# Kernel optimization log

Hardware: AMD Instinct MI355X
Metric: run time of the kernel (lower is better)

Reference implementation:

```python
import jax, jax.numpy as jnp
import numpy as np

DIM = 512
HEADS = 8


def setup_inputs() -> dict:
    key = jax.random.key(0)
    ks = jax.random.split(key, 9)
    s = 1.0 / np.sqrt(DIM)
    x = jax.random.normal(ks[0], (2, 4096, DIM), dtype=jnp.float32)
    Wq = jax.random.uniform(ks[1], (DIM, DIM), jnp.float32, -s, s)
    bq = jax.random.uniform(ks[2], (DIM,), jnp.float32, -s, s)
    Wk = jax.random.uniform(ks[3], (DIM, DIM), jnp.float32, -s, s)
    bk = jax.random.uniform(ks[4], (DIM,), jnp.float32, -s, s)
    Wv = jax.random.uniform(ks[5], (DIM, DIM), jnp.float32, -s, s)
    bv = jax.random.uniform(ks[6], (DIM,), jnp.float32, -s, s)
    Wo = jax.random.uniform(ks[7], (DIM, DIM), jnp.float32, -s, s)
    bo = jax.random.uniform(ks[8], (DIM,), jnp.float32, -s, s)
    return {"x": x, "Wq": Wq, "bq": bq, "Wk": Wk, "bk": bk,
            "Wv": Wv, "bv": bv, "Wo": Wo, "bo": bo}


def reference(x, Wq, bq, Wk, bk, Wv, bv, Wo, bo):
    b, t, d = x.shape
    h = HEADS
    dq = d // h
    scale = dq ** -0.5
    # projections: torch Linear is x @ W.T + b
    q = (x @ Wq.T + bq).reshape(b, t, h, dq)
    k = (x @ Wk.T + bk).reshape(b, t, h, dq)
    v = (x @ Wv.T + bv).reshape(b, t, h, dq)
    # attention scores [b, h, t, t] (full O(T^2) matrix, as in the original)
    att = jnp.einsum("bqhd,bkhd->bhqk", q, k) * scale
    att = jax.nn.softmax(att, axis=-1)
    out = jnp.einsum("bhqk,bkhd->bqhd", att, v).reshape(b, t, d)
    return out @ Wo.T + bo
```

## Files before the change

### kernel.cpp

```cpp
#include <hip/hip_runtime.h>

typedef short bf16x8 __attribute__((ext_vector_type(8)));
typedef float f32x4 __attribute__((ext_vector_type(4)));

#define MFMA(a, b, c) __builtin_amdgcn_mfma_f32_16x16x32_bf16((a), (b), (c), 0, 0, 0)

__device__ __forceinline__ unsigned short f2bf(float f) {
    unsigned u = __builtin_bit_cast(unsigned, f);
    unsigned r = u + 0x7FFFu + ((u >> 16) & 1u);
    return (unsigned short)(r >> 16);
}
__device__ __forceinline__ unsigned rne2(float a, float b) {
    unsigned ua = __builtin_bit_cast(unsigned, a);
    unsigned ub = __builtin_bit_cast(unsigned, b);
    ua += 0x7FFFu + ((ua >> 16) & 1u);
    ub += 0x7FFFu + ((ub >> 16) & 1u);
    return __builtin_amdgcn_perm(ub, ua, 0x07060302u);
}

__global__ __launch_bounds__(256) void cvt_kernel(
    const float* __restrict__ x,
    const float* __restrict__ w0, const float* __restrict__ w1,
    const float* __restrict__ w2, const float* __restrict__ w3,
    unsigned short* __restrict__ xd,
    unsigned short* __restrict__ d0, unsigned short* __restrict__ d1,
    unsigned short* __restrict__ d2, unsigned short* __restrict__ d3)
{
    int bid = blockIdx.x;
    const float* src;
    unsigned short* dst;
    int off;
    if (bid < 4096) { src = x; dst = xd; off = bid; }
    else {
        int s = (bid - 4096) >> 8;
        src = s == 0 ? w0 : (s == 1 ? w1 : (s == 2 ? w2 : w3));
        dst = s == 0 ? d0 : (s == 1 ? d1 : (s == 2 ? d2 : d3));
        off = (bid - 4096) & 255;
    }
    size_t i = ((size_t)off * 256 + threadIdx.x) * 4;
    float4 v = *(const float4*)(src + i);
    uint2 pk;
    pk.x = rne2(v.x, v.y);
    pk.y = rne2(v.z, v.w);
    *(uint2*)(dst + i) = pk;
}

__device__ __forceinline__ void gemm128_core(
    const unsigned short* __restrict__ A, const unsigned short* __restrict__ W,
    int m0, int n0, int tid, unsigned short* sA, unsigned short* sB,
    f32x4 acc[4][4])
{
    const int lane = tid & 63, wid = tid >> 6;
    const int quad = lane >> 4, l15 = lane & 15;
    const int wm = wid >> 1, wn = wid & 1;

    #pragma unroll
    for (int i = 0; i < 4; i++)
        #pragma unroll
        for (int j = 0; j < 4; j++) {
            f32x4 z = {0.f, 0.f, 0.f, 0.f};
            acc[i][j] = z;
        }

    for (int k0 = 0; k0 < 512; k0 += 64) {
        #pragma unroll
        for (int p = 0; p < 4; p++) {
            int c = tid + p * 256;
            int row = c >> 3, kc = c & 7;
            uint4 va = *(const uint4*)(A + (size_t)(m0 + row) * 512 + k0 + kc * 8);
            *(uint4*)((char*)sA + row * 128 + ((kc ^ (row & 7)) << 4)) = va;
            uint4 vb = *(const uint4*)(W + (size_t)(n0 + row) * 512 + k0 + kc * 8);
            *(uint4*)((char*)sB + row * 128 + ((kc ^ (row & 7)) << 4)) = vb;
        }
        __syncthreads();
        #pragma unroll
        for (int ks = 0; ks < 2; ks++) {
            bf16x8 af[4], bfr[4];
            #pragma unroll
            for (int i = 0; i < 4; i++) {
                int row = wm * 64 + i * 16 + l15;
                int kc = ks * 4 + quad;
                af[i] = *(const bf16x8*)((const char*)sA + row * 128 + ((kc ^ (row & 7)) << 4));
            }
            #pragma unroll
            for (int j = 0; j < 4; j++) {
                int row = wn * 64 + j * 16 + l15;
                int kc = ks * 4 + quad;
                bfr[j] = *(const bf16x8*)((const char*)sB + row * 128 + ((kc ^ (row & 7)) << 4));
            }
            #pragma unroll
            for (int i = 0; i < 4; i++)
                #pragma unroll
                for (int j = 0; j < 4; j++)
                    acc[i][j] = MFMA(af[i], bfr[j], acc[i][j]);
        }
        __syncthreads();
    }
}

__global__ __launch_bounds__(256) void qkv_kernel(
    const unsigned short* __restrict__ x,
    const unsigned short* __restrict__ Wq, const float* __restrict__ bq,
    const unsigned short* __restrict__ Wk, const float* __restrict__ bk,
    const unsigned short* __restrict__ Wv, const float* __restrict__ bv,
    unsigned short* __restrict__ qo, unsigned short* __restrict__ ko,
    unsigned short* __restrict__ vo)
{
    __shared__ unsigned short sA[128 * 64];
    __shared__ unsigned short sB[128 * 64];
    const int tid = threadIdx.x;
    const int by = blockIdx.y;
    const int sel = by >> 2;
    const int n0 = (by & 3) * 128;
    const int m0 = blockIdx.x * 128;
    const unsigned short* W = sel == 0 ? Wq : (sel == 1 ? Wk : Wv);
    const float* bias = sel == 0 ? bq : (sel == 1 ? bk : bv);

    f32x4 acc[4][4];
    gemm128_core(x, W, m0, n0, tid, sA, sB, acc);

    const int lane = tid & 63, wid = tid >> 6;
    const int quad = lane >> 4, l15 = lane & 15;
    const int wm = wid >> 1, wn = wid & 1;
    float bv4[4];
    #pragma unroll
    for (int j = 0; j < 4; j++) bv4[j] = bias[n0 + wn * 64 + j * 16 + l15];

    if (sel == 2) {
        #pragma unroll
        for (int i = 0; i < 4; i++) {
            #pragma unroll
            for (int j = 0; j < 4; j++) {
                int n = n0 + wn * 64 + j * 16 + l15;
                int h = n >> 6, d = n & 63;
                int m = m0 + wm * 64 + i * 16 + quad * 4;
                int b = m >> 12, t = m & 4095;
                uint2 pk;
                pk.x = rne2(acc[i][j][0] + bv4[j], acc[i][j][1] + bv4[j]);
                pk.y = rne2(acc[i][j][2] + bv4[j], acc[i][j][3] + bv4[j]);
                *(uint2*)(vo + ((size_t)(b * 8 + h) * 64 + d) * 4096 + t) = pk;
            }
        }
    } else {
        const float SC = (sel == 0) ? 0.125f * 1.44269504088896f : 1.0f;
        unsigned short* dst = sel == 0 ? qo : ko;
        #pragma unroll
        for (int i = 0; i < 4; i++) {
            #pragma unroll
            for (int j = 0; j < 4; j++) {
                int n = n0 + wn * 64 + j * 16 + l15;
                int h = n >> 6, d = n & 63;
                #pragma unroll
                for (int r = 0; r < 4; r++) {
                    int m = m0 + wm * 64 + i * 16 + quad * 4 + r;
                    int b = m >> 12, t = m & 4095;
                    dst[((size_t)(b * 8 + h) * 4096 + t) * 64 + d] =
                        f2bf((acc[i][j][r] + bv4[j]) * SC);
                }
            }
        }
    }
}

__global__ __launch_bounds__(512, 4) void attn_kernel(
    const unsigned short* __restrict__ qg, const unsigned short* __restrict__ kg,
    const unsigned short* __restrict__ vtg, unsigned short* __restrict__ og)
{
    __shared__ unsigned char smem[65536];

    const int tid = threadIdx.x;
    const int lane = tid & 63;
    const int w = tid >> 6;
    const int g = tid >> 8;
    const int gt = tid & 255;
    const int sw = w & 3;
    const int quad = lane >> 4, l15 = lane & 15;
    const int bh = blockIdx.y;
    const size_t base = (size_t)bh * 4096 * 64;
    const unsigned short* Q = qg + base;
    const unsigned short* K = kg + base;
    const unsigned short* VT = vtg + base;
    const int qt0 = blockIdx.x * 128;

    unsigned short* sK  = (unsigned short*)(smem + g * 8192);
    unsigned short* sVt = (unsigned short*)(smem + 16384 + g * 8192);
    unsigned char*  sP  = smem + 32768 + w * 4096;

    bf16x8 qf[2][2];
    #pragma unroll
    for (int cb = 0; cb < 2; cb++) {
        int q = qt0 + sw * 32 + cb * 16 + l15;
        #pragma unroll
        for (int ks = 0; ks < 2; ks++)
            qf[cb][ks] = *(const bf16x8*)(Q + (size_t)q * 64 + ks * 32 + quad * 8);
    }

    f32x4 ot[4][2];
    #pragma unroll
    for (int i = 0; i < 4; i++)
        #pragma unroll
        for (int cb = 0; cb < 2; cb++) {
            f32x4 z = {0.f, 0.f, 0.f, 0.f};
            ot[i][cb] = z;
        }
    f32x4 ls[2];
    {
        f32x4 z = {0.f, 0.f, 0.f, 0.f};
        ls[0] = z; ls[1] = z;
    }
    const short one_b = (short)0x3F80;
    const bf16x8 ones = {one_b, one_b, one_b, one_b, one_b, one_b, one_b, one_b};

    const int c0 = gt, c1 = gt + 256;
    const int r0 = c0 >> 3, kc0 = c0 & 7;
    const int r1 = c1 >> 3, kc1 = c1 & 7;

    uint4 kr0, kr1, vr0, vr1;
    {
        int kb = g * 64;
        kr0 = *(const uint4*)(K + (size_t)(kb + r0) * 64 + kc0 * 8);
        kr1 = *(const uint4*)(K + (size_t)(kb + r1) * 64 + kc1 * 8);
        vr0 = *(const uint4*)(VT + (size_t)r0 * 4096 + kb + kc0 * 8);
        vr1 = *(const uint4*)(VT + (size_t)r1 * 4096 + kb + kc1 * 8);
    }

    for (int it = 0; it < 32; it++) {
        *(uint4*)((char*)sK + r0 * 128 + ((kc0 ^ (r0 & 7)) << 4)) = kr0;
        *(uint4*)((char*)sK + r1 * 128 + ((kc1 ^ (r1 & 7)) << 4)) = kr1;
        *(uint4*)((char*)sVt + r0 * 128 + ((kc0 ^ (r0 & 7)) << 4)) = vr0;
        *(uint4*)((char*)sVt + r1 * 128 + ((kc1 ^ (r1 & 7)) << 4)) = vr1;
        __syncthreads();

        {
            int itn = (it < 31) ? it + 1 : it;
            int kbn = (2 * itn + g) * 64;
            kr0 = *(const uint4*)(K + (size_t)(kbn + r0) * 64 + kc0 * 8);
            kr1 = *(const uint4*)(K + (size_t)(kbn + r1) * 64 + kc1 * 8);
            vr0 = *(const uint4*)(VT + (size_t)r0 * 4096 + kbn + kc0 * 8);
            vr1 = *(const uint4*)(VT + (size_t)r1 * 4096 + kbn + kc1 * 8);
        }

        #pragma unroll
        for (int rb = 0; rb < 4; rb++) {
            int row = rb * 16 + l15;
            f32x4 s0 = {0.f, 0.f, 0.f, 0.f};
            f32x4 s1 = {0.f, 0.f, 0.f, 0.f};
            #pragma unroll
            for (int ks = 0; ks < 2; ks++) {
                int kc = ks * 4 + quad;
                bf16x8 ka = *(const bf16x8*)((const char*)sK + row * 128 + ((kc ^ (row & 7)) << 4));
                s0 = MFMA(ka, qf[0][ks], s0);
                s1 = MFMA(ka, qf[1][ks], s1);
            }
            int poff = (((rb * 2 + (quad >> 1)) ^ (l15 & 7)) << 4) + ((quad & 1) << 3);
            {
                float p0 = __builtin_amdgcn_exp2f(s0[0]);
                float p1 = __builtin_amdgcn_exp2f(s0[1]);
                float p2 = __builtin_amdgcn_exp2f(s0[2]);
                float p3 = __builtin_amdgcn_exp2f(s0[3]);
                uint2 pk;
                pk.x = rne2(p0, p1);
                pk.y = rne2(p2, p3);
                *(uint2*)(sP + l15 * 128 + poff) = pk;
            }
            {
                float p0 = __builtin_amdgcn_exp2f(s1[0]);
                float p1 = __builtin_amdgcn_exp2f(s1[1]);
                float p2 = __builtin_amdgcn_exp2f(s1[2]);
                float p3 = __builtin_amdgcn_exp2f(s1[3]);
                uint2 pk;
                pk.x = rne2(p0, p1);
                pk.y = rne2(p2, p3);
                *(uint2*)(sP + (16 + l15) * 128 + poff) = pk;
            }
        }
        __asm__ __volatile__("s_waitcnt lgkmcnt(0)" ::: "memory");

        #pragma unroll
        for (int ks2 = 0; ks2 < 2; ks2++) {
            int pslot = (((ks2 * 4 + quad) ^ (l15 & 7)) << 4);
            bf16x8 pfr0 = *(const bf16x8*)(sP + l15 * 128 + pslot);
            bf16x8 pfr1 = *(const bf16x8*)(sP + (16 + l15) * 128 + pslot);
            ls[0] = MFMA(ones, pfr0, ls[0]);
            ls[1] = MFMA(ones, pfr1, ls[1]);
            #pragma unroll
            for (int rbd = 0; rbd < 4; rbd++) {
                int row = rbd * 16 + l15;
                int kc = ks2 * 4 + quad;
                bf16x8 vf = *(const bf16x8*)((const char*)sVt + row * 128 + ((kc ^ (row & 7)) << 4));
                ot[rbd][0] = MFMA(vf, pfr0, ot[rbd][0]);
                ot[rbd][1] = MFMA(vf, pfr1, ot[rbd][1]);
            }
        }
        __syncthreads();
    }

    float* oc = (float*)(smem + 32768);
    float* lc = (float*)smem;
    if (g == 1) {
        #pragma unroll
        for (int cb = 0; cb < 2; cb++) {
            int qb = sw * 32 + cb * 16 + l15;
            if (quad == 0) lc[qb] = ls[cb][0];
            #pragma unroll
            for (int rbd = 0; rbd < 4; rbd++) {
                int dc = rbd * 4 + quad;
                *(f32x4*)((char*)oc + qb * 256 + ((dc ^ (qb & 15)) << 4)) = ot[rbd][cb];
            }
        }
    }
    __syncthreads();
    if (g == 0) {
        const int b = bh >> 3, h = bh & 7;
        #pragma unroll
        for (int cb = 0; cb < 2; cb++) {
            int qb = sw * 32 + cb * 16 + l15;
            float inv = 1.f / (ls[cb][0] + lc[qb]);
            int q = qt0 + qb;
            #pragma unroll
            for (int rbd = 0; rbd < 4; rbd++) {
                int dc = rbd * 4 + quad;
                f32x4 o2 = *(const f32x4*)((char*)oc + qb * 256 + ((dc ^ (qb & 15)) << 4));
                float v0 = (ot[rbd][cb][0] + o2[0]) * inv;
                float v1 = (ot[rbd][cb][1] + o2[1]) * inv;
                float v2 = (ot[rbd][cb][2] + o2[2]) * inv;
                float v3 = (ot[rbd][cb][3] + o2[3]) * inv;
                uint2 pk;
                pk.x = rne2(v0, v1);
                pk.y = rne2(v2, v3);
                *(uint2*)(og + ((size_t)(b * 4096 + q) * 512 + h * 64 + rbd * 16 + quad * 4)) = pk;
            }
        }
    }
}

__global__ __launch_bounds__(256) void out_kernel(
    const unsigned short* __restrict__ attn,
    const unsigned short* __restrict__ Wo, const float* __restrict__ bo,
    float* __restrict__ out)
{
    __shared__ unsigned short sA[128 * 64];
    __shared__ unsigned short sB[128 * 64];
    const int tid = threadIdx.x;
    const int m0 = blockIdx.x * 128;
    const int n0 = blockIdx.y * 128;

    f32x4 acc[4][4];
    gemm128_core(attn, Wo, m0, n0, tid, sA, sB, acc);

    const int lane = tid & 63, wid = tid >> 6;
    const int quad = lane >> 4, l15 = lane & 15;
    const int wm = wid >> 1, wn = wid & 1;
    float bv4[4];
    #pragma unroll
    for (int j = 0; j < 4; j++) bv4[j] = bo[n0 + wn * 64 + j * 16 + l15];
    #pragma unroll
    for (int i = 0; i < 4; i++) {
        #pragma unroll
        for (int j = 0; j < 4; j++) {
            int n = n0 + wn * 64 + j * 16 + l15;
            #pragma unroll
            for (int r = 0; r < 4; r++) {
                int m = m0 + wm * 64 + i * 16 + quad * 4 + r;
                out[(size_t)m * 512 + n] = acc[i][j][r] + bv4[j];
            }
        }
    }
}

extern "C" void kernel_launch(void* const* d_in, const int* in_sizes, int n_in,
                              void* d_out, int out_size, void* d_ws, size_t ws_size,
                              hipStream_t stream) {
    const float* x  = (const float*)d_in[0];
    const float* Wq = (const float*)d_in[1];
    const float* bq = (const float*)d_in[2];
    const float* Wk = (const float*)d_in[3];
    const float* bk = (const float*)d_in[4];
    const float* Wv = (const float*)d_in[5];
    const float* bv = (const float*)d_in[6];
    const float* Wo = (const float*)d_in[7];
    const float* bo = (const float*)d_in[8];
    unsigned short* ws = (unsigned short*)d_ws;

    const size_t NTOK = (size_t)2 * 4096 * 512;
    const size_t WSZ = (size_t)512 * 512;
    unsigned short* xb  = ws;
    unsigned short* Wqb = ws + NTOK;
    unsigned short* Wkb = Wqb + WSZ;
    unsigned short* Wvb = Wkb + WSZ;
    unsigned short* Wob = Wvb + WSZ;
    unsigned short* q_ws = Wob + WSZ;
    unsigned short* k_ws = q_ws + NTOK;
    unsigned short* v_ws = k_ws + NTOK;
    unsigned short* a_ws = v_ws + NTOK;

    cvt_kernel<<<5120, 256, 0, stream>>>(x, Wq, Wk, Wv, Wo, xb, Wqb, Wkb, Wvb, Wob);
    qkv_kernel<<<dim3(64, 12), 256, 0, stream>>>(xb, Wqb, bq, Wkb, bk, Wvb, bv,
                                                 q_ws, k_ws, v_ws);
    attn_kernel<<<dim3(32, 16), 512, 0, stream>>>(q_ws, k_ws, v_ws, a_ws);
    out_kernel<<<dim3(64, 4), 256, 0, stream>>>(a_ws, Wob, bo,
                                                (float*)d_out);
}
```

Measured before the change: 206.3 us.

## Fuse x fp32-to-bf16 conversion into QKV GEMM and vectorize epilogue stores

```diff
diff --git a/kernel.cpp b/kernel.cpp
--- a/kernel.cpp
+++ b/kernel.cpp
@@ -5,39 +5,40 @@
 
 #define MFMA(a, b, c) __builtin_amdgcn_mfma_f32_16x16x32_bf16((a), (b), (c), 0, 0, 0)
 
-__device__ __forceinline__ unsigned short f2bf(float f) {
-    unsigned u = __builtin_bit_cast(unsigned, f);
-    unsigned r = u + 0x7FFFu + ((u >> 16) & 1u);
-    return (unsigned short)(r >> 16);
-}
 __device__ __forceinline__ unsigned rne2(float a, float b) {
+#if __has_builtin(__builtin_amdgcn_cvt_pk_bf16_f32)
+    auto v = __builtin_amdgcn_cvt_pk_bf16_f32(a, b);
+    return __builtin_bit_cast(unsigned, v);
+#else
     unsigned ua = __builtin_bit_cast(unsigned, a);
     unsigned ub = __builtin_bit_cast(unsigned, b);
     ua += 0x7FFFu + ((ua >> 16) & 1u);
     ub += 0x7FFFu + ((ub >> 16) & 1u);
     return __builtin_amdgcn_perm(ub, ua, 0x07060302u);
+#endif
+}
+
+__device__ __forceinline__ uint4 cvt8(const float* __restrict__ p) {
+    float4 a = *(const float4*)p;
+    float4 b = *(const float4*)(p + 4);
+    uint4 r;
+    r.x = rne2(a.x, a.y);
+    r.y = rne2(a.z, a.w);
+    r.z = rne2(b.x, b.y);
+    r.w = rne2(b.z, b.w);
+    return r;
 }
 
 __global__ __launch_bounds__(256) void cvt_kernel(
-    const float* __restrict__ x,
     const float* __restrict__ w0, const float* __restrict__ w1,
     const float* __restrict__ w2, const float* __restrict__ w3,
-    unsigned short* __restrict__ xd,
     unsigned short* __restrict__ d0, unsigned short* __restrict__ d1,
     unsigned short* __restrict__ d2, unsigned short* __restrict__ d3)
 {
-    int bid = blockIdx.x;
-    const float* src;
-    unsigned short* dst;
-    int off;
-    if (bid < 4096) { src = x; dst = xd; off = bid; }
-    else {
-        int s = (bid - 4096) >> 8;
-        src = s == 0 ? w0 : (s == 1 ? w1 : (s == 2 ? w2 : w3));
-        dst = s == 0 ? d0 : (s == 1 ? d1 : (s == 2 ? d2 : d3));
-        off = (bid - 4096) & 255;
-    }
-    size_t i = ((size_t)off * 256 + threadIdx.x) * 4;
+    int s = blockIdx.x >> 8;
+    const float* src = s == 0 ? w0 : (s == 1 ? w1 : (s == 2 ? w2 : w3));
+    unsigned short* dst = s == 0 ? d0 : (s == 1 ? d1 : (s == 2 ? d2 : d3));
+    size_t i = ((size_t)(blockIdx.x & 255) * 256 + threadIdx.x) * 4;
     float4 v = *(const float4*)(src + i);
     uint2 pk;
     pk.x = rne2(v.x, v.y);
@@ -45,9 +46,10 @@
     *(uint2*)(dst + i) = pk;
 }
 
+template<bool AF32, bool BF32>
 __device__ __forceinline__ void gemm128_core(
-    const unsigned short* __restrict__ A, const unsigned short* __restrict__ W,
-    int m0, int n0, int tid, unsigned short* sA, unsigned short* sB,
+    const void* __restrict__ A, const void* __restrict__ B,
+    int a0, int b0, int tid, unsigned short* sA, unsigned short* sB,
     f32x4 acc[4][4])
 {
     const int lane = tid & 63, wid = tid >> 6;
@@ -67,9 +69,12 @@
         for (int p = 0; p < 4; p++) {
             int c = tid + p * 256;
             int row = c >> 3, kc = c & 7;
-            uint4 va = *(const uint4*)(A + (size_t)(m0 + row) * 512 + k0 + kc * 8);
+            uint4 va, vb;
+            if (AF32) va = cvt8((const float*)A + (size_t)(a0 + row) * 512 + k0 + kc * 8);
+            else      va = *(const uint4*)((const unsigned short*)A + (size_t)(a0 + row) * 512 + k0 + kc * 8);
+            if (BF32) vb = cvt8((const float*)B + (size_t)(b0 + row) * 512 + k0 + kc * 8);
+            else      vb = *(const uint4*)((const unsigned short*)B + (size_t)(b0 + row) * 512 + k0 + kc * 8);
             *(uint4*)((char*)sA + row * 128 + ((kc ^ (row & 7)) << 4)) = va;
-            uint4 vb = *(const uint4*)(W + (size_t)(n0 + row) * 512 + k0 + kc * 8);
             *(uint4*)((char*)sB + row * 128 + ((kc ^ (row & 7)) << 4)) = vb;
         }
         __syncthreads();
@@ -99,7 +104,7 @@
 }
 
 __global__ __launch_bounds__(256) void qkv_kernel(
-    const unsigned short* __restrict__ x,
+    const float* __restrict__ x,
     const unsigned short* __restrict__ Wq, const float* __restrict__ bq,
     const unsigned short* __restrict__ Wk, const float* __restrict__ bk,
     const unsigned short* __restrict__ Wv, const float* __restrict__ bv,
@@ -109,24 +114,22 @@
     __shared__ unsigned short sA[128 * 64];
     __shared__ unsigned short sB[128 * 64];
     const int tid = threadIdx.x;
-    const int by = blockIdx.y;
-    const int sel = by >> 2;
-    const int n0 = (by & 3) * 128;
-    const int m0 = blockIdx.x * 128;
-    const unsigned short* W = sel == 0 ? Wq : (sel == 1 ? Wk : Wv);
-    const float* bias = sel == 0 ? bq : (sel == 1 ? bk : bv);
-
-    f32x4 acc[4][4];
-    gemm128_core(x, W, m0, n0, tid, sA, sB, acc);
+    const int bx = blockIdx.x;
+    const int sel = bx >> 2;
+    const int n0 = (bx & 3) * 128;
+    const int m0 = blockIdx.y * 128;
 
     const int lane = tid & 63, wid = tid >> 6;
     const int quad = lane >> 4, l15 = lane & 15;
     const int wm = wid >> 1, wn = wid & 1;
-    float bv4[4];
-    #pragma unroll
-    for (int j = 0; j < 4; j++) bv4[j] = bias[n0 + wn * 64 + j * 16 + l15];
+
+    f32x4 acc[4][4];
 
     if (sel == 2) {
+        gemm128_core<true, false>(x, Wv, m0, n0, tid, sA, sB, acc);
+        float bv4[4];
+        #pragma unroll
+        for (int j = 0; j < 4; j++) bv4[j] = bv[n0 + wn * 64 + j * 16 + l15];
         #pragma unroll
         for (int i = 0; i < 4; i++) {
             #pragma unroll
@@ -142,21 +145,24 @@
             }
         }
     } else {
+        const unsigned short* W = sel == 0 ? Wq : Wk;
+        const float* bias = sel == 0 ? bq : bk;
+        unsigned short* dst = sel == 0 ? qo : ko;
         const float SC = (sel == 0) ? 0.125f * 1.44269504088896f : 1.0f;
-        unsigned short* dst = sel == 0 ? qo : ko;
+        gemm128_core<false, true>(W, x, n0, m0, tid, sA, sB, acc);
         #pragma unroll
         for (int i = 0; i < 4; i++) {
+            int nb = n0 + wm * 64 + i * 16 + quad * 4;
+            int h = nb >> 6, d0 = nb & 63;
+            f32x4 bb = *(const f32x4*)(bias + nb);
             #pragma unroll
             for (int j = 0; j < 4; j++) {
-                int n = n0 + wn * 64 + j * 16 + l15;
-                int h = n >> 6, d = n & 63;
-                #pragma unroll
-                for (int r = 0; r < 4; r++) {
-                    int m = m0 + wm * 64 + i * 16 + quad * 4 + r;
-                    int b = m >> 12, t = m & 4095;
-                    dst[((size_t)(b * 8 + h) * 4096 + t) * 64 + d] =
-                        f2bf((acc[i][j][r] + bv4[j]) * SC);
-                }
+                int m = m0 + wn * 64 + j * 16 + l15;
+                int b = m >> 12, t = m & 4095;
+                uint2 pk;
+                pk.x = rne2((acc[i][j][0] + bb[0]) * SC, (acc[i][j][1] + bb[1]) * SC);
+                pk.y = rne2((acc[i][j][2] + bb[2]) * SC, (acc[i][j][3] + bb[3]) * SC);
+                *(uint2*)(dst + ((size_t)(b * 8 + h) * 4096 + t) * 64 + d0) = pk;
             }
         }
     }
@@ -342,28 +348,28 @@
     __shared__ unsigned short sA[128 * 64];
     __shared__ unsigned short sB[128 * 64];
     const int tid = threadIdx.x;
-    const int m0 = blockIdx.x * 128;
-    const int n0 = blockIdx.y * 128;
+    const int n0 = blockIdx.x * 128;
+    const int m0 = blockIdx.y * 128;
 
     f32x4 acc[4][4];
-    gemm128_core(attn, Wo, m0, n0, tid, sA, sB, acc);
+    gemm128_core<false, false>(Wo, attn, n0, m0, tid, sA, sB, acc);
 
     const int lane = tid & 63, wid = tid >> 6;
     const int quad = lane >> 4, l15 = lane & 15;
     const int wm = wid >> 1, wn = wid & 1;
-    float bv4[4];
-    #pragma unroll
-    for (int j = 0; j < 4; j++) bv4[j] = bo[n0 + wn * 64 + j * 16 + l15];
     #pragma unroll
     for (int i = 0; i < 4; i++) {
+        int nb = n0 + wm * 64 + i * 16 + quad * 4;
+        f32x4 bb = *(const f32x4*)(bo + nb);
         #pragma unroll
         for (int j = 0; j < 4; j++) {
-            int n = n0 + wn * 64 + j * 16 + l15;
-            #pragma unroll
-            for (int r = 0; r < 4; r++) {
-                int m = m0 + wm * 64 + i * 16 + quad * 4 + r;
-                out[(size_t)m * 512 + n] = acc[i][j][r] + bv4[j];
-            }
+            int m = m0 + wn * 64 + j * 16 + l15;
+            f32x4 v;
+            v[0] = acc[i][j][0] + bb[0];
+            v[1] = acc[i][j][1] + bb[1];
+            v[2] = acc[i][j][2] + bb[2];
+            v[3] = acc[i][j][3] + bb[3];
+            *(f32x4*)(out + (size_t)m * 512 + nb) = v;
         }
     }
 }
@@ -384,8 +390,7 @@
 
     const size_t NTOK = (size_t)2 * 4096 * 512;
     const size_t WSZ = (size_t)512 * 512;
-    unsigned short* xb  = ws;
-    unsigned short* Wqb = ws + NTOK;
+    unsigned short* Wqb = ws;
     unsigned short* Wkb = Wqb + WSZ;
     unsigned short* Wvb = Wkb + WSZ;
     unsigned short* Wob = Wvb + WSZ;
@@ -394,10 +399,10 @@
     unsigned short* v_ws = k_ws + NTOK;
     unsigned short* a_ws = v_ws + NTOK;
 
-    cvt_kernel<<<5120, 256, 0, stream>>>(x, Wq, Wk, Wv, Wo, xb, Wqb, Wkb, Wvb, Wob);
-    qkv_kernel<<<dim3(64, 12), 256, 0, stream>>>(xb, Wqb, bq, Wkb, bk, Wvb, bv,
+    cvt_kernel<<<1024, 256, 0, stream>>>(Wq, Wk, Wv, Wo, Wqb, Wkb, Wvb, Wob);
+    qkv_kernel<<<dim3(12, 64), 256, 0, stream>>>(x, Wqb, bq, Wkb, bk, Wvb, bv,
                                                  q_ws, k_ws, v_ws);
     attn_kernel<<<dim3(32, 16), 512, 0, stream>>>(q_ws, k_ws, v_ws, a_ws);
-    out_kernel<<<dim3(64, 4), 256, 0, stream>>>(a_ws, Wob, bo,
+    out_kernel<<<dim3(4, 64), 256, 0, stream>>>(a_ws, Wob, bo,
                                                 (float*)d_out);
 }
```

Measured after the change: 216.3 us. +4.9%, slower.

## Halve attention block to 4 waves, each covering 64 queries for more K/V reuse

Applied to the files above, without the earlier changes.

```diff
diff --git a/kernel.cpp b/kernel.cpp
--- a/kernel.cpp
+++ b/kernel.cpp
@@ -11,11 +11,16 @@
     return (unsigned short)(r >> 16);
 }
 __device__ __forceinline__ unsigned rne2(float a, float b) {
+#if __has_builtin(__builtin_amdgcn_cvt_pk_bf16_f32)
+    auto v = __builtin_amdgcn_cvt_pk_bf16_f32(a, b);
+    return __builtin_bit_cast(unsigned, v);
+#else
     unsigned ua = __builtin_bit_cast(unsigned, a);
     unsigned ub = __builtin_bit_cast(unsigned, b);
     ua += 0x7FFFu + ((ua >> 16) & 1u);
     ub += 0x7FFFu + ((ub >> 16) & 1u);
     return __builtin_amdgcn_perm(ub, ua, 0x07060302u);
+#endif
 }
 
 __global__ __launch_bounds__(256) void cvt_kernel(
@@ -162,7 +167,7 @@
     }
 }
 
-__global__ __launch_bounds__(512, 4) void attn_kernel(
+__global__ __launch_bounds__(256, 2) void attn_kernel(
     const unsigned short* __restrict__ qg, const unsigned short* __restrict__ kg,
     const unsigned short* __restrict__ vtg, unsigned short* __restrict__ og)
 {
@@ -171,9 +176,8 @@
     const int tid = threadIdx.x;
     const int lane = tid & 63;
     const int w = tid >> 6;
-    const int g = tid >> 8;
-    const int gt = tid & 255;
-    const int sw = w & 3;
+    const int g = w >> 1;
+    const int sw = w & 1;
     const int quad = lane >> 4, l15 = lane & 15;
     const int bh = blockIdx.y;
     const size_t base = (size_t)bh * 4096 * 64;
@@ -184,112 +188,116 @@
 
     unsigned short* sK  = (unsigned short*)(smem + g * 8192);
     unsigned short* sVt = (unsigned short*)(smem + 16384 + g * 8192);
-    unsigned char*  sP  = smem + 32768 + w * 4096;
-
-    bf16x8 qf[2][2];
-    #pragma unroll
-    for (int cb = 0; cb < 2; cb++) {
-        int q = qt0 + sw * 32 + cb * 16 + l15;
+    unsigned char*  sP  = smem + 32768 + w * 8192;
+
+    bf16x8 qf[4][2];
+    #pragma unroll
+    for (int cb = 0; cb < 4; cb++) {
+        int q = qt0 + sw * 64 + cb * 16 + l15;
         #pragma unroll
         for (int ks = 0; ks < 2; ks++)
             qf[cb][ks] = *(const bf16x8*)(Q + (size_t)q * 64 + ks * 32 + quad * 8);
     }
 
-    f32x4 ot[4][2];
+    f32x4 ot[4][4];
     #pragma unroll
     for (int i = 0; i < 4; i++)
         #pragma unroll
-        for (int cb = 0; cb < 2; cb++) {
+        for (int cb = 0; cb < 4; cb++) {
             f32x4 z = {0.f, 0.f, 0.f, 0.f};
             ot[i][cb] = z;
         }
-    f32x4 ls[2];
-    {
+    f32x4 ls[4];
+    #pragma unroll
+    for (int cb = 0; cb < 4; cb++) {
         f32x4 z = {0.f, 0.f, 0.f, 0.f};
-        ls[0] = z; ls[1] = z;
+        ls[cb] = z;
     }
     const short one_b = (short)0x3F80;
     const bf16x8 ones = {one_b, one_b, one_b, one_b, one_b, one_b, one_b, one_b};
 
-    const int c0 = gt, c1 = gt + 256;
-    const int r0 = c0 >> 3, kc0 = c0 & 7;
-    const int r1 = c1 >> 3, kc1 = c1 & 7;
-
-    uint4 kr0, kr1, vr0, vr1;
+    const int r_lo = tid >> 3, r_hi = 32 + (tid >> 3), kc = tid & 7;
+    const int swz_lo = ((kc ^ (r_lo & 7)) << 4);
+
+    uint4 kr0, kr1, kr2, kr3, vr0, vr1, vr2, vr3;
     {
-        int kb = g * 64;
-        kr0 = *(const uint4*)(K + (size_t)(kb + r0) * 64 + kc0 * 8);
-        kr1 = *(const uint4*)(K + (size_t)(kb + r1) * 64 + kc1 * 8);
-        vr0 = *(const uint4*)(VT + (size_t)r0 * 4096 + kb + kc0 * 8);
-        vr1 = *(const uint4*)(VT + (size_t)r1 * 4096 + kb + kc1 * 8);
+        int kb0 = 0, kb1 = 64;
+        kr0 = *(const uint4*)(K + (size_t)(kb0 + r_lo) * 64 + kc * 8);
+        kr1 = *(const uint4*)(K + (size_t)(kb0 + r_hi) * 64 + kc * 8);
+        kr2 = *(const uint4*)(K + (size_t)(kb1 + r_lo) * 64 + kc * 8);
+        kr3 = *(const uint4*)(K + (size_t)(kb1 + r_hi) * 64 + kc * 8);
+        vr0 = *(const uint4*)(VT + (size_t)r_lo * 4096 + kb0 + kc * 8);
+        vr1 = *(const uint4*)(VT + (size_t)r_hi * 4096 + kb0 + kc * 8);
+        vr2 = *(const uint4*)(VT + (size_t)r_lo * 4096 + kb1 + kc * 8);
+        vr3 = *(const uint4*)(VT + (size_t)r_hi * 4096 + kb1 + kc * 8);
     }
 
     for (int it = 0; it < 32; it++) {
-        *(uint4*)((char*)sK + r0 * 128 + ((kc0 ^ (r0 & 7)) << 4)) = kr0;
-        *(uint4*)((char*)sK + r1 * 128 + ((kc1 ^ (r1 & 7)) << 4)) = kr1;
-        *(uint4*)((char*)sVt + r0 * 128 + ((kc0 ^ (r0 & 7)) << 4)) = vr0;
-        *(uint4*)((char*)sVt + r1 * 128 + ((kc1 ^ (r1 & 7)) << 4)) = vr1;
+        *(uint4*)(smem + r_lo * 128 + swz_lo) = kr0;
+        *(uint4*)(smem + r_hi * 128 + swz_lo) = kr1;
+        *(uint4*)(smem + 8192 + r_lo * 128 + swz_lo) = kr2;
+        *(uint4*)(smem + 8192 + r_hi * 128 + swz_lo) = kr3;
+        *(uint4*)(smem + 16384 + r_lo * 128 + swz_lo) = vr0;
+        *(uint4*)(smem + 16384 + r_hi * 128 + swz_lo) = vr1;
+        *(uint4*)(smem + 24576 + r_lo * 128 + swz_lo) = vr2;
+        *(uint4*)(smem + 24576 + r_hi * 128 + swz_lo) = vr3;
         __syncthreads();
 
         {
             int itn = (it < 31) ? it + 1 : it;
-            int kbn = (2 * itn + g) * 64;
-            kr0 = *(const uint4*)(K + (size_t)(kbn + r0) * 64 + kc0 * 8);
-            kr1 = *(const uint4*)(K + (size_t)(kbn + r1) * 64 + kc1 * 8);
-            vr0 = *(const uint4*)(VT + (size_t)r0 * 4096 + kbn + kc0 * 8);
-            vr1 = *(const uint4*)(VT + (size_t)r1 * 4096 + kbn + kc1 * 8);
+            int kb0 = (2 * itn) * 64, kb1 = (2 * itn + 1) * 64;
+            kr0 = *(const uint4*)(K + (size_t)(kb0 + r_lo) * 64 + kc * 8);
+            kr1 = *(const uint4*)(K + (size_t)(kb0 + r_hi) * 64 + kc * 8);
+            kr2 = *(const uint4*)(K + (size_t)(kb1 + r_lo) * 64 + kc * 8);
+            kr3 = *(const uint4*)(K + (size_t)(kb1 + r_hi) * 64 + kc * 8);
+            vr0 = *(const uint4*)(VT + (size_t)r_lo * 4096 + kb0 + kc * 8);
+            vr1 = *(const uint4*)(VT + (size_t)r_hi * 4096 + kb0 + kc * 8);
+            vr2 = *(const uint4*)(VT + (size_t)r_lo * 4096 + kb1 + kc * 8);
+            vr3 = *(const uint4*)(VT + (size_t)r_hi * 4096 + kb1 + kc * 8);
         }
 
         #pragma unroll
         for (int rb = 0; rb < 4; rb++) {
             int row = rb * 16 + l15;
-            f32x4 s0 = {0.f, 0.f, 0.f, 0.f};
-            f32x4 s1 = {0.f, 0.f, 0.f, 0.f};
-            #pragma unroll
-            for (int ks = 0; ks < 2; ks++) {
-                int kc = ks * 4 + quad;
-                bf16x8 ka = *(const bf16x8*)((const char*)sK + row * 128 + ((kc ^ (row & 7)) << 4));
-                s0 = MFMA(ka, qf[0][ks], s0);
-                s1 = MFMA(ka, qf[1][ks], s1);
-            }
+            bf16x8 ka0 = *(const bf16x8*)((const char*)sK + row * 128 + (((0 + quad) ^ (row & 7)) << 4));
+            bf16x8 ka1 = *(const bf16x8*)((const char*)sK + row * 128 + (((4 + quad) ^ (row & 7)) << 4));
             int poff = (((rb * 2 + (quad >> 1)) ^ (l15 & 7)) << 4) + ((quad & 1) << 3);
-            {
-                float p0 = __builtin_amdgcn_exp2f(s0[0]);
-                float p1 = __builtin_amdgcn_exp2f(s0[1]);
-                float p2 = __builtin_amdgcn_exp2f(s0[2]);
-                float p3 = __builtin_amdgcn_exp2f(s0[3]);
+            #pragma unroll
+            for (int cb = 0; cb < 4; cb++) {
+                f32x4 s = {0.f, 0.f, 0.f, 0.f};
+                s = MFMA(ka0, qf[cb][0], s);
+                s = MFMA(ka1, qf[cb][1], s);
+                float p0 = __builtin_amdgcn_exp2f(s[0]);
+                float p1 = __builtin_amdgcn_exp2f(s[1]);
+                float p2 = __builtin_amdgcn_exp2f(s[2]);
+                float p3 = __builtin_amdgcn_exp2f(s[3]);
                 uint2 pk;
                 pk.x = rne2(p0, p1);
                 pk.y = rne2(p2, p3);
-                *(uint2*)(sP + l15 * 128 + poff) = pk;
-            }
-            {
-                float p0 = __builtin_amdgcn_exp2f(s1[0]);
-                float p1 = __builtin_amdgcn_exp2f(s1[1]);
-                float p2 = __builtin_amdgcn_exp2f(s1[2]);
-                float p3 = __builtin_amdgcn_exp2f(s1[3]);
-                uint2 pk;
-                pk.x = rne2(p0, p1);
-                pk.y = rne2(p2, p3);
-                *(uint2*)(sP + (16 + l15) * 128 + poff) = pk;
+                *(uint2*)(sP + (cb * 16 + l15) * 128 + poff) = pk;
             }
         }
         __asm__ __volatile__("s_waitcnt lgkmcnt(0)" ::: "memory");
 
         #pragma unroll
         for (int ks2 = 0; ks2 < 2; ks2++) {
-            int pslot = (((ks2 * 4 + quad) ^ (l15 & 7)) << 4);
-            bf16x8 pfr0 = *(const bf16x8*)(sP + l15 * 128 + pslot);
-            bf16x8 pfr1 = *(const bf16x8*)(sP + (16 + l15) * 128 + pslot);
-            ls[0] = MFMA(ones, pfr0, ls[0]);
-            ls[1] = MFMA(ones, pfr1, ls[1]);
+            bf16x8 pfr[4];
+            #pragma unroll
+            for (int cb = 0; cb < 4; cb++) {
+                int pslot = (((ks2 * 4 + quad) ^ (l15 & 7)) << 4);
+                pfr[cb] = *(const bf16x8*)(sP + (cb * 16 + l15) * 128 + pslot);
+            }
+            #pragma unroll
+            for (int cb = 0; cb < 4; cb++)
+                ls[cb] = MFMA(ones, pfr[cb], ls[cb]);
             #pragma unroll
             for (int rbd = 0; rbd < 4; rbd++) {
                 int row = rbd * 16 + l15;
-                int kc = ks2 * 4 + quad;
-                bf16x8 vf = *(const bf16x8*)((const char*)sVt + row * 128 + ((kc ^ (row & 7)) << 4));
-                ot[rbd][0] = MFMA(vf, pfr0, ot[rbd][0]);
-                ot[rbd][1] = MFMA(vf, pfr1, ot[rbd][1]);
+                int kcv = ks2 * 4 + quad;
+                bf16x8 vf = *(const bf16x8*)((const char*)sVt + row * 128 + ((kcv ^ (row & 7)) << 4));
+                #pragma unroll
+                for (int cb = 0; cb < 4; cb++)
+                    ot[rbd][cb] = MFMA(vf, pfr[cb], ot[rbd][cb]);
             }
         }
         __syncthreads();
@@ -299,8 +307,8 @@
     float* lc = (float*)smem;
     if (g == 1) {
         #pragma unroll
-        for (int cb = 0; cb < 2; cb++) {
-            int qb = sw * 32 + cb * 16 + l15;
+        for (int cb = 0; cb < 4; cb++) {
+            int qb = sw * 64 + cb * 16 + l15;
             if (quad == 0) lc[qb] = ls[cb][0];
             #pragma unroll
             for (int rbd = 0; rbd < 4; rbd++) {
@@ -313,8 +321,8 @@
     if (g == 0) {
         const int b = bh >> 3, h = bh & 7;
         #pragma unroll
-        for (int cb = 0; cb < 2; cb++) {
-            int qb = sw * 32 + cb * 16 + l15;
+        for (int cb = 0; cb < 4; cb++) {
+            int qb = sw * 64 + cb * 16 + l15;
             float inv = 1.f / (ls[cb][0] + lc[qb]);
             int q = qt0 + qb;
             #pragma unroll
@@ -397,7 +405,7 @@
     cvt_kernel<<<5120, 256, 0, stream>>>(x, Wq, Wk, Wv, Wo, xb, Wqb, Wkb, Wvb, Wob);
     qkv_kernel<<<dim3(64, 12), 256, 0, stream>>>(xb, Wqb, bq, Wkb, bk, Wvb, bv,
                                                  q_ws, k_ws, v_ws);
-    attn_kernel<<<dim3(32, 16), 512, 0, stream>>>(q_ws, k_ws, v_ws, a_ws);
+    attn_kernel<<<dim3(32, 16), 256, 0, stream>>>(q_ws, k_ws, v_ws, a_ws);
     out_kernel<<<dim3(64, 4), 256, 0, stream>>>(a_ws, Wob, bo,
                                                 (float*)d_out);
 }
```

Measured after the change: 211.8 us. 1.03x slower.

## Keep softmax probabilities in registers and feed PV with 16x16x16 MFMA

Applied to the files above, without the earlier changes.

```diff
diff --git a/kernel.cpp b/kernel.cpp
--- a/kernel.cpp
+++ b/kernel.cpp
@@ -1,9 +1,22 @@
 #include <hip/hip_runtime.h>
 
 typedef short bf16x8 __attribute__((ext_vector_type(8)));
+typedef short bf16x4 __attribute__((ext_vector_type(4)));
 typedef float f32x4 __attribute__((ext_vector_type(4)));
 
 #define MFMA(a, b, c) __builtin_amdgcn_mfma_f32_16x16x32_bf16((a), (b), (c), 0, 0, 0)
+
+#if __has_builtin(__builtin_amdgcn_mfma_f32_16x16x16bf16_1k)
+__device__ __forceinline__ f32x4 mfma16(bf16x4 a, bf16x4 b, f32x4 c) {
+    return __builtin_amdgcn_mfma_f32_16x16x16bf16_1k(a, b, c, 0, 0, 0);
+}
+#else
+__device__ __forceinline__ f32x4 mfma16(bf16x4 a, bf16x4 b, f32x4 c) {
+    bf16x8 a8 = {a[0], a[1], a[2], a[3], 0, 0, 0, 0};
+    bf16x8 b8 = {b[0], b[1], b[2], b[3], 0, 0, 0, 0};
+    return MFMA(a8, b8, c);
+}
+#endif
 
 __device__ __forceinline__ unsigned short f2bf(float f) {
     unsigned u = __builtin_bit_cast(unsigned, f);
@@ -11,11 +24,16 @@
     return (unsigned short)(r >> 16);
 }
 __device__ __forceinline__ unsigned rne2(float a, float b) {
+#if __has_builtin(__builtin_amdgcn_cvt_pk_bf16_f32)
+    auto v = __builtin_amdgcn_cvt_pk_bf16_f32(a, b);
+    return __builtin_bit_cast(unsigned, v);
+#else
     unsigned ua = __builtin_bit_cast(unsigned, a);
     unsigned ub = __builtin_bit_cast(unsigned, b);
     ua += 0x7FFFu + ((ua >> 16) & 1u);
     ub += 0x7FFFu + ((ub >> 16) & 1u);
     return __builtin_amdgcn_perm(ub, ua, 0x07060302u);
+#endif
 }
 
 __global__ __launch_bounds__(256) void cvt_kernel(
@@ -166,12 +184,12 @@
     const unsigned short* __restrict__ qg, const unsigned short* __restrict__ kg,
     const unsigned short* __restrict__ vtg, unsigned short* __restrict__ og)
 {
-    __shared__ unsigned char smem[65536];
+    __shared__ unsigned char smem[33280];
 
     const int tid = threadIdx.x;
     const int lane = tid & 63;
     const int w = tid >> 6;
-    const int g = tid >> 8;
+    const int g = w >> 2;
     const int gt = tid & 255;
     const int sw = w & 3;
     const int quad = lane >> 4, l15 = lane & 15;
@@ -184,7 +202,6 @@
 
     unsigned short* sK  = (unsigned short*)(smem + g * 8192);
     unsigned short* sVt = (unsigned short*)(smem + 16384 + g * 8192);
-    unsigned char*  sP  = smem + 32768 + w * 4096;
 
     bf16x8 qf[2][2];
     #pragma unroll
@@ -209,94 +226,74 @@
         ls[0] = z; ls[1] = z;
     }
     const short one_b = (short)0x3F80;
-    const bf16x8 ones = {one_b, one_b, one_b, one_b, one_b, one_b, one_b, one_b};
-
-    const int c0 = gt, c1 = gt + 256;
-    const int r0 = c0 >> 3, kc0 = c0 & 7;
-    const int r1 = c1 >> 3, kc1 = c1 & 7;
+    const bf16x4 ones = {one_b, one_b, one_b, one_b};
+
+    const int r0 = gt >> 3, r1 = 32 + (gt >> 3), kc = gt & 7;
+    const int swz = ((kc ^ (r0 & 7)) << 4);
 
     uint4 kr0, kr1, vr0, vr1;
     {
         int kb = g * 64;
-        kr0 = *(const uint4*)(K + (size_t)(kb + r0) * 64 + kc0 * 8);
-        kr1 = *(const uint4*)(K + (size_t)(kb + r1) * 64 + kc1 * 8);
-        vr0 = *(const uint4*)(VT + (size_t)r0 * 4096 + kb + kc0 * 8);
-        vr1 = *(const uint4*)(VT + (size_t)r1 * 4096 + kb + kc1 * 8);
+        kr0 = *(const uint4*)(K + (size_t)(kb + r0) * 64 + kc * 8);
+        kr1 = *(const uint4*)(K + (size_t)(kb + r1) * 64 + kc * 8);
+        vr0 = *(const uint4*)(VT + (size_t)r0 * 4096 + kb + kc * 8);
+        vr1 = *(const uint4*)(VT + (size_t)r1 * 4096 + kb + kc * 8);
     }
 
     for (int it = 0; it < 32; it++) {
-        *(uint4*)((char*)sK + r0 * 128 + ((kc0 ^ (r0 & 7)) << 4)) = kr0;
-        *(uint4*)((char*)sK + r1 * 128 + ((kc1 ^ (r1 & 7)) << 4)) = kr1;
-        *(uint4*)((char*)sVt + r0 * 128 + ((kc0 ^ (r0 & 7)) << 4)) = vr0;
-        *(uint4*)((char*)sVt + r1 * 128 + ((kc1 ^ (r1 & 7)) << 4)) = vr1;
+        *(uint4*)((char*)sK + r0 * 128 + swz) = kr0;
+        *(uint4*)((char*)sK + r1 * 128 + swz) = kr1;
+        *(uint4*)((char*)sVt + r0 * 128 + swz) = vr0;
+        *(uint4*)((char*)sVt + r1 * 128 + swz) = vr1;
         __syncthreads();
 
         {
             int itn = (it < 31) ? it + 1 : it;
             int kbn = (2 * itn + g) * 64;
-            kr0 = *(const uint4*)(K + (size_t)(kbn + r0) * 64 + kc0 * 8);
-            kr1 = *(const uint4*)(K + (size_t)(kbn + r1) * 64 + kc1 * 8);
-            vr0 = *(const uint4*)(VT + (size_t)r0 * 4096 + kbn + kc0 * 8);
-            vr1 = *(const uint4*)(VT + (size_t)r1 * 4096 + kbn + kc1 * 8);
+            kr0 = *(const uint4*)(K + (size_t)(kbn + r0) * 64 + kc * 8);
+            kr1 = *(const uint4*)(K + (size_t)(kbn + r1) * 64 + kc * 8);
+            vr0 = *(const uint4*)(VT + (size_t)r0 * 4096 + kbn + kc * 8);
+            vr1 = *(const uint4*)(VT + (size_t)r1 * 4096 + kbn + kc * 8);
         }
 
         #pragma unroll
         for (int rb = 0; rb < 4; rb++) {
             int row = rb * 16 + l15;
-            f32x4 s0 = {0.f, 0.f, 0.f, 0.f};
-            f32x4 s1 = {0.f, 0.f, 0.f, 0.f};
-            #pragma unroll
-            for (int ks = 0; ks < 2; ks++) {
-                int kc = ks * 4 + quad;
-                bf16x8 ka = *(const bf16x8*)((const char*)sK + row * 128 + ((kc ^ (row & 7)) << 4));
-                s0 = MFMA(ka, qf[0][ks], s0);
-                s1 = MFMA(ka, qf[1][ks], s1);
-            }
-            int poff = (((rb * 2 + (quad >> 1)) ^ (l15 & 7)) << 4) + ((quad & 1) << 3);
-            {
-                float p0 = __builtin_amdgcn_exp2f(s0[0]);
-                float p1 = __builtin_amdgcn_exp2f(s0[1]);
-                float p2 = __builtin_amdgcn_exp2f(s0[2]);
-                float p3 = __builtin_amdgcn_exp2f(s0[3]);
+            bf16x8 ka0 = *(const bf16x8*)((const char*)sK + row * 128 + (((0 + quad) ^ (row & 7)) << 4));
+            bf16x8 ka1 = *(const bf16x8*)((const char*)sK + row * 128 + (((4 + quad) ^ (row & 7)) << 4));
+            bf16x4 pb[2];
+            #pragma unroll
+            for (int cb = 0; cb < 2; cb++) {
+                f32x4 s = {0.f, 0.f, 0.f, 0.f};
+                s = MFMA(ka0, qf[cb][0], s);
+                s = MFMA(ka1, qf[cb][1], s);
+                float p0 = __builtin_amdgcn_exp2f(s[0]);
+                float p1 = __builtin_amdgcn_exp2f(s[1]);
+                float p2 = __builtin_amdgcn_exp2f(s[2]);
+                float p3 = __builtin_amdgcn_exp2f(s[3]);
                 uint2 pk;
                 pk.x = rne2(p0, p1);
                 pk.y = rne2(p2, p3);
-                *(uint2*)(sP + l15 * 128 + poff) = pk;
-            }
-            {
-                float p0 = __builtin_amdgcn_exp2f(s1[0]);
-                float p1 = __builtin_amdgcn_exp2f(s1[1]);
-                float p2 = __builtin_amdgcn_exp2f(s1[2]);
-                float p3 = __builtin_amdgcn_exp2f(s1[3]);
-                uint2 pk;
-                pk.x = rne2(p0, p1);
-                pk.y = rne2(p2, p3);
-                *(uint2*)(sP + (16 + l15) * 128 + poff) = pk;
-            }
-        }
-        __asm__ __volatile__("s_waitcnt lgkmcnt(0)" ::: "memory");
-
-        #pragma unroll
-        for (int ks2 = 0; ks2 < 2; ks2++) {
-            int pslot = (((ks2 * 4 + quad) ^ (l15 & 7)) << 4);
-            bf16x8 pfr0 = *(const bf16x8*)(sP + l15 * 128 + pslot);
-            bf16x8 pfr1 = *(const bf16x8*)(sP + (16 + l15) * 128 + pslot);
-            ls[0] = MFMA(ones, pfr0, ls[0]);
-            ls[1] = MFMA(ones, pfr1, ls[1]);
+                pb[cb] = __builtin_bit_cast(bf16x4, pk);
+            }
+            ls[0] = mfma16(ones, pb[0], ls[0]);
+            ls[1] = mfma16(ones, pb[1], ls[1]);
+            int vcol = (((rb * 2 + (quad >> 1))) << 4) + ((quad & 1) << 3);
             #pragma unroll
             for (int rbd = 0; rbd < 4; rbd++) {
-                int row = rbd * 16 + l15;
-                int kc = ks2 * 4 + quad;
-                bf16x8 vf = *(const bf16x8*)((const char*)sVt + row * 128 + ((kc ^ (row & 7)) << 4));
-                ot[rbd][0] = MFMA(vf, pfr0, ot[rbd][0]);
-                ot[rbd][1] = MFMA(vf, pfr1, ot[rbd][1]);
-            }
+                int d = rbd * 16 + l15;
+                int chunk = (rb * 2 + (quad >> 1)) ^ (d & 7);
+                bf16x4 vf = *(const bf16x4*)((const char*)sVt + d * 128 + (chunk << 4) + ((quad & 1) << 3));
+                ot[rbd][0] = mfma16(vf, pb[0], ot[rbd][0]);
+                ot[rbd][1] = mfma16(vf, pb[1], ot[rbd][1]);
+            }
+            (void)vcol;
         }
         __syncthreads();
     }
 
-    float* oc = (float*)(smem + 32768);
-    float* lc = (float*)smem;
+    float* oc = (float*)smem;
+    float* lc = (float*)(smem + 32768);
     if (g == 1) {
         #pragma unroll
         for (int cb = 0; cb < 2; cb++) {
```

New measurement: 209.2 us. No clear change (+1.4%).
